# Kernel optimization log

Hardware: AMD Instinct MI355X
Metric: run time of the kernel (lower is better)

The kernel has to match this reference:

```python
import jax, jax.numpy as jnp
import numpy as np
from jax import lax

THRESHOLD = 10.0


def _conv(x, w):
    # x: [N,1,H,W], w: [O,1,kh,kw], SAME padding, stride 1 (matches nn.Conv2d with symmetric padding)
    return lax.conv_general_dilated(x, w, window_strides=(1, 1), padding='SAME',
                                    dimension_numbers=('NCHW', 'OIHW', 'NCHW'))


def _make_filters():
    # scipy.signal.gaussian(5, std=1.0): unnormalized gaussian window
    gauss = np.exp(-0.5 * ((np.arange(5) - 2.0) ** 2)).astype(np.float32)
    gauss_w = gauss.reshape(1, 1, 1, 5)  # horizontal 1x5 filter
    sobel = np.array([[1, 0, -1], [2, 0, -2], [1, 0, -1]], np.float32)
    sobel_x = sobel[None, None]  # [1,1,3,3]
    f0 = [[0, 0, 0], [0, 1, -1], [0, 0, 0]]
    f45 = [[0, 0, 0], [0, 1, 0], [0, 0, -1]]
    f90 = [[0, 0, 0], [0, 1, 0], [0, -1, 0]]
    f135 = [[0, 0, 0], [0, 1, 0], [-1, 0, 0]]
    f180 = [[0, 0, 0], [-1, 1, 0], [0, 0, 0]]
    f225 = [[-1, 0, 0], [0, 1, 0], [0, 0, 0]]
    f270 = [[0, -1, 0], [0, 1, 0], [0, 0, 0]]
    f315 = [[0, 0, -1], [0, 1, 0], [0, 0, 0]]
    dir_w = np.stack([f0, f45, f90, f135, f180, f225, f270, f315]).astype(np.float32)[:, None]  # [8,1,3,3]
    return jnp.asarray(gauss_w), jnp.asarray(sobel_x), jnp.asarray(dir_w)


def setup_inputs() -> dict:
    key = jax.random.key(0)
    B, H, W = 4, 1024, 1024
    img = jax.random.uniform(key, (B, 3, H, W), dtype=jnp.float32) * 255.0  # pixel-scale values
    gauss_w, sobel_x, dir_w = _make_filters()
    return {'img': img, 'gauss_w': gauss_w, 'sobel_x': sobel_x, 'dir_w': dir_w}


def reference(img, gauss_w, sobel_x, dir_w):
    B, C, H, W = img.shape  # C == 3
    x = img.reshape(B * 3, 1, H, W)
    # Separable gaussian blur (horizontal then vertical), all 3 channels batched together
    blurred = _conv(_conv(x, gauss_w), jnp.transpose(gauss_w, (0, 1, 3, 2)))  # [B*3,1,H,W]
    # Sobel gradients per channel
    gx = _conv(blurred, sobel_x).reshape(B, 3, H, W)
    gy = _conv(blurred, jnp.transpose(sobel_x, (0, 1, 3, 2))).reshape(B, 3, H, W)
    # Magnitude: sum of per-channel L2 magnitudes
    grad_mag = jnp.sum(jnp.sqrt(gx * gx + gy * gy), axis=1, keepdims=True)  # [B,1,H,W]
    # Orientation from summed gradients, quantized to 45-degree bins (same pi constant as original)
    grad_orientation = jnp.arctan2(gy.sum(1, keepdims=True), gx.sum(1, keepdims=True)) * (180.0 / 3.14159)
    grad_orientation = jnp.round((grad_orientation + 180.0) / 45.0) * 45.0
    # Directional differences for non-max suppression
    all_filtered = _conv(grad_mag, dir_w)  # [B,8,H,W]
    idx_pos = ((grad_orientation / 45.0) % 8).astype(jnp.int32)          # [B,1,H,W]
    idx_neg = ((grad_orientation / 45.0 + 4.0) % 8).astype(jnp.int32)
    pos = jnp.take_along_axis(all_filtered, idx_pos, axis=1)  # [B,1,H,W]
    neg = jnp.take_along_axis(all_filtered, idx_neg, axis=1)
    is_max = jnp.minimum(pos, neg) > 0.0
    thin_edges = jnp.where(is_max, grad_mag, 0.0)
    thresholded = jnp.where(thin_edges < THRESHOLD, 0.0, thin_edges)
    early_threshold = jnp.where(grad_mag < THRESHOLD, 0.0, grad_mag)
    blurred_img = blurred.reshape(B, 3, H, W)[None]  # matches torch.stack([squeeze(...)]) for B>1
    return (blurred_img, grad_mag, grad_orientation, thin_edges, thresholded, early_threshold)
```

## Files before the change

### kernel.cpp

```cpp
#include <hip/hip_runtime.h>
#include <math.h>


#define OUTW 56
#define ROWS 8
#define NT   256

struct TrigC { double c0,s0,c1,s1,c2,s2,c3,s3; };

struct ChS {
    double hA,hB,hC,hD;
    double d0,d1;
    double v0,v1;
    float  rwP;
};

__global__ __launch_bounds__(NT, 2) void canny_wave_kernel(
    const float* __restrict__ img,
    const float* __restrict__ gauss,
    float* __restrict__ out_blur,
    float* __restrict__ out_mag,
    float* __restrict__ out_ori,
    float* __restrict__ out_thin,
    float* __restrict__ out_thr,
    float* __restrict__ out_early,
    TrigC tc, int H, int W)
{
    const int lane  = threadIdx.x & 63;
    const int wid   = threadIdx.x >> 6;
    const int strip = blockIdx.x;
    const int seg   = blockIdx.y * 4 + wid;
    const int b     = blockIdx.z;

    const int  x   = strip * OUTW + lane - 4;
    const bool xin = (unsigned)x < (unsigned)W;
    const int  r0  = seg * ROWS;

    const double g0 = (double)gauss[0], g1 = (double)gauss[1], g2 = (double)gauss[2];
    const size_t cs = (size_t)H * W;
    const float* ip0 = img + (size_t)(b * 3 + 0) * cs;
    const float* ip1 = ip0 + cs;
    const float* ip2 = ip1 + cs;
    float* bp0 = out_blur + (size_t)(b * 3 + 0) * cs;
    float* bp1 = bp0 + cs;
    float* bp2 = bp1 + cs;

    const bool outok = xin && lane >= 4 && lane <= 59;

    auto rawload = [&](const float* ip, int y) -> float {
        return (xin && (unsigned)y < (unsigned)H) ? ip[(size_t)y * W + x] : 0.f;
    };
    auto hconv = [&](float rw) -> double {
        float m2 = __shfl(rw, lane - 2);
        float m1 = __shfl(rw, lane - 1);
        float p1 = __shfl(rw, lane + 1);
        float p2 = __shfl(rw, lane + 2);
        return g0 * ((double)m2 + (double)p2) + g1 * ((double)m1 + (double)p1)
             + g2 * (double)rw;
    };
    auto hinit = [&](const float* ip, ChS& s) {
        s.hA = hconv(rawload(ip, r0 - 4));
        s.hB = hconv(rawload(ip, r0 - 3));
        s.hC = hconv(rawload(ip, r0 - 2));
        s.hD = hconv(rawload(ip, r0 - 1));
        s.d0 = 0.0; s.d1 = 0.0; s.v0 = 0.0; s.v1 = 0.0;
        s.rwP = rawload(ip, r0);
    };
    auto chstep = [&](const float* ip, float* bp, ChS& s, int v,
                      double& msum, double& gxs, double& gys) {
        float  rw = s.rwP;
        s.rwP = rawload(ip, v + 3);
        double hE = hconv(rw);
        double vbn = g0 * (s.hA + hE) + g1 * (s.hB + s.hD) + g2 * s.hC;
        if (!xin || (unsigned)v >= (unsigned)H) vbn = 0.0;
        if (v >= r0 && v < r0 + ROWS && outok)
            bp[(size_t)v * W + x] = (float)vbn;
        double vbL = __shfl(vbn, lane - 1), vbR = __shfl(vbn, lane + 1);
        double dn = vbL - vbR;
        double cc = s.v0 - vbn;
        double cL = __shfl(cc, lane - 1), cR = __shfl(cc, lane + 1);
        double gx = s.d0 + 2.0 * s.d1 + dn;
        double gy = cL + 2.0 * cc + cR;
        msum += sqrt(gx * gx + gy * gy);
        gxs += gx; gys += gy;
        s.hA = s.hB; s.hB = s.hC; s.hC = s.hD; s.hD = hE;
        s.d0 = s.d1; s.d1 = dn;
        s.v0 = s.v1; s.v1 = vbn;
    };

    ChS c0s, c1s, c2s;
    hinit(ip0, c0s); hinit(ip1, c1s); hinit(ip2, c2s);

    double mg0 = 0.0, mg1 = 0.0, mgL0 = 0.0, mgL1 = 0.0, mgR0 = 0.0, mgR1 = 0.0;
    double gxp = 0.0, gyp = 0.0;
    const size_t ob = (size_t)b * cs;

    for (int v = r0 - 2; v <= r0 + ROWS + 1; ++v) {
        double msum = 0.0, gxn = 0.0, gyn = 0.0;
        chstep(ip0, bp0, c0s, v, msum, gxn, gyn);
        chstep(ip1, bp1, c1s, v, msum, gxn, gyn);
        chstep(ip2, bp2, c2s, v, msum, gxn, gyn);
        const int m = v - 1;
        const bool mv = ((unsigned)m < (unsigned)H) && xin && lane >= 3 && lane <= 60;
        double magn = mv ? msum : 0.0;
        double mgLn = __shfl(magn, lane - 1);
        double mgRn = __shfl(magn, lane + 1);

        if (v >= r0 + 2 && outok) {
            const int r = v - 2;
            double m_c = mg1;
            double gxv = gxp, gyv = gyp;

            double a = fabs(gyv);
            int n = (int)(a * tc.c0 - gxv * tc.s0 >= 0.0)
                  + (int)(a * tc.c1 - gxv * tc.s1 >= 0.0)
                  + (int)(a * tc.c2 - gxv * tc.s2 >= 0.0)
                  + (int)(a * tc.c3 - gxv * tc.s3 >= 0.0);
            int k;
            if (gyv == 0.0) {
                bool gxneg = signbit(gxv);
                k = signbit(gyv) ? (gxneg ? 0 : 4) : (gxneg ? 8 : 4);
            } else {
                k = signbit(gyv) ? 4 - n : 4 + n;
            }
            float q = 45.f * (float)k;
            if (gxv < 0.0 && fabs(gyv) < 1e-2) q = 180.f;

            int kp = k & 7;
            int dy = (int)((0x00012221u >> (kp * 4)) & 7u) - 1;
            int dx = (int)((0x21000122u >> (kp * 4)) & 7u) - 1;

            double rL = (dy < 0) ? mgL0 : (dy > 0 ? mgLn : mgL1);
            double rC = (dy < 0) ? mg0  : (dy > 0 ? magn : mg1);
            double rR = (dy < 0) ? mgR0 : (dy > 0 ? mgRn : mgR1);
            double posn = (dx < 0) ? rL : (dx > 0 ? rR : rC);
            double sL = (dy > 0) ? mgL0 : (dy < 0 ? mgLn : mgL1);
            double sC = (dy > 0) ? mg0  : (dy < 0 ? magn : mg1);
            double sR = (dy > 0) ? mgR0 : (dy < 0 ? mgRn : mgR1);
            double negn = (dx > 0) ? sL : (dx < 0 ? sR : sC);

            double pos = m_c - posn;
            double neg = m_c - negn;
            float mf = (float)m_c;
            float thin = (fmin(pos, neg) > 0.0) ? mf : 0.f;
            size_t idx = ob + (size_t)r * W + x;
            out_mag[idx]   = mf;
            out_ori[idx]   = q;
            out_thin[idx]  = thin;
            out_thr[idx]   = (thin < 10.f) ? 0.f : thin;
            out_early[idx] = (mf < 10.f) ? 0.f : mf;
        }

        mg0 = mg1; mg1 = magn;
        mgL0 = mgL1; mgL1 = mgLn;
        mgR0 = mgR1; mgR1 = mgRn;
        gxp = gxn; gyp = gyn;
    }
}

extern "C" void kernel_launch(void* const* d_in, const int* in_sizes, int n_in,
                              void* d_out, int out_size, void* d_ws, size_t ws_size,
                              hipStream_t stream) {
    const float* img   = (const float*)d_in[0];
    const float* gauss = (const float*)d_in[1];
    const int H = 1024, W = 1024;
    const int B = in_sizes[0] / (3 * H * W);

    float* out = (float*)d_out;
    const size_t cs = (size_t)H * W;
    float* out_blur  = out;
    float* out_mag   = out_blur + (size_t)B * 3 * cs;
    float* out_ori   = out_mag  + (size_t)B * cs;
    float* out_thin  = out_ori  + (size_t)B * cs;
    float* out_thr   = out_thin + (size_t)B * cs;
    float* out_early = out_thr  + (size_t)B * cs;

    const double C = 180.0 / 3.14159;
    TrigC tc;
    { double bta = 22.5 / C;  tc.c0 = cos(bta); tc.s0 = sin(bta); }
    { double bta = 67.5 / C;  tc.c1 = cos(bta); tc.s1 = sin(bta); }
    { double bta = 112.5 / C; tc.c2 = cos(bta); tc.s2 = sin(bta); }
    { double bta = 157.5 / C; tc.c3 = cos(bta); tc.s3 = sin(bta); }

    dim3 grid((W + OUTW - 1) / OUTW, H / (ROWS * 4), B);
    canny_wave_kernel<<<grid, NT, 0, stream>>>(
        img, gauss, out_blur, out_mag, out_ori, out_thin, out_thr, out_early, tc, H, W);
}
```

Baseline: 89.71 us.

## Process two adjacent pixels per lane with float2 loads and stores

Each lane now handles a horizontal pair of pixels, so a wave covers 120 output columns instead of 56. The overlapping halo work and shuffles per output pixel both shrink, and all global loads and stores become float2 vector accesses. The cost is roughly double the per-lane register state (double-precision histories for both pixels), which may hurt occupancy or cause spills. There is also a leftover redundant dn0 assignment.

```diff
diff --git a/kernel.cpp b/kernel.cpp
--- a/kernel.cpp
+++ b/kernel.cpp
@@ -2,17 +2,17 @@
 #include <math.h>
 
 
-#define OUTW 56
+#define PW   120
 #define ROWS 8
 #define NT   256
 
 struct TrigC { double c0,s0,c1,s1,c2,s2,c3,s3; };
 
 struct ChS {
-    double hA,hB,hC,hD;
-    double d0,d1;
-    double v0,v1;
-    float  rwP;
+    double hAa,hBa,hCa,hDa, hAb,hBb,hCb,hDb;
+    double d0a,d1a, d0b,d1b;
+    double v0a,v1a, v0b,v1b;
+    float  rw0,rw1;
 };
 
 __global__ __launch_bounds__(NT, 2) void canny_wave_kernel(
@@ -32,9 +32,10 @@
     const int seg   = blockIdx.y * 4 + wid;
     const int b     = blockIdx.z;
 
-    const int  x   = strip * OUTW + lane - 4;
-    const bool xin = (unsigned)x < (unsigned)W;
-    const int  r0  = seg * ROWS;
+    const int x0 = strip * PW - 4 + 2 * lane;
+    const int x1 = x0 + 1;
+    const bool pairok = (x0 >= 0) && (x1 < W);
+    const int  r0 = seg * ROWS;
 
     const double g0 = (double)gauss[0], g1 = (double)gauss[1], g2 = (double)gauss[2];
     const size_t cs = (size_t)H * W;
@@ -45,116 +46,149 @@
     float* bp1 = bp0 + cs;
     float* bp2 = bp1 + cs;
 
-    const bool outok = xin && lane >= 4 && lane <= 59;
-
-    auto rawload = [&](const float* ip, int y) -> float {
-        return (xin && (unsigned)y < (unsigned)H) ? ip[(size_t)y * W + x] : 0.f;
-    };
-    auto hconv = [&](float rw) -> double {
-        float m2 = __shfl(rw, lane - 2);
-        float m1 = __shfl(rw, lane - 1);
-        float p1 = __shfl(rw, lane + 1);
-        float p2 = __shfl(rw, lane + 2);
-        return g0 * ((double)m2 + (double)p2) + g1 * ((double)m1 + (double)p1)
-             + g2 * (double)rw;
+    const bool outok = (lane >= 2) && (lane <= 61) && ((unsigned)x0 < (unsigned)W);
+
+    auto rawload2 = [&](const float* ip, int y, float& o0, float& o1) {
+        if ((unsigned)y < (unsigned)H) {
+            if (pairok) {
+                float2 t = *reinterpret_cast<const float2*>(ip + (size_t)y * W + x0);
+                o0 = t.x; o1 = t.y;
+            } else {
+                o0 = ((unsigned)x0 < (unsigned)W) ? ip[(size_t)y * W + x0] : 0.f;
+                o1 = ((unsigned)x1 < (unsigned)W) ? ip[(size_t)y * W + x1] : 0.f;
+            }
+        } else { o0 = 0.f; o1 = 0.f; }
+    };
+    auto hpair = [&](float w0, float w1, double& hh0, double& hh1) {
+        float am0 = __shfl(w0, lane - 1), am1 = __shfl(w1, lane - 1);
+        float ap0 = __shfl(w0, lane + 1), ap1 = __shfl(w1, lane + 1);
+        hh0 = g0 * ((double)am0 + (double)ap0) + g1 * ((double)am1 + (double)w1) + g2 * (double)w0;
+        hh1 = g0 * ((double)am1 + (double)ap1) + g1 * ((double)w0 + (double)ap0) + g2 * (double)w1;
     };
     auto hinit = [&](const float* ip, ChS& s) {
-        s.hA = hconv(rawload(ip, r0 - 4));
-        s.hB = hconv(rawload(ip, r0 - 3));
-        s.hC = hconv(rawload(ip, r0 - 2));
-        s.hD = hconv(rawload(ip, r0 - 1));
-        s.d0 = 0.0; s.d1 = 0.0; s.v0 = 0.0; s.v1 = 0.0;
-        s.rwP = rawload(ip, r0);
+        float w0, w1;
+        rawload2(ip, r0 - 4, w0, w1); hpair(w0, w1, s.hAa, s.hAb);
+        rawload2(ip, r0 - 3, w0, w1); hpair(w0, w1, s.hBa, s.hBb);
+        rawload2(ip, r0 - 2, w0, w1); hpair(w0, w1, s.hCa, s.hCb);
+        rawload2(ip, r0 - 1, w0, w1); hpair(w0, w1, s.hDa, s.hDb);
+        s.d0a = s.d1a = s.d0b = s.d1b = 0.0;
+        s.v0a = s.v1a = s.v0b = s.v1b = 0.0;
+        rawload2(ip, r0, s.rw0, s.rw1);
     };
     auto chstep = [&](const float* ip, float* bp, ChS& s, int v,
-                      double& msum, double& gxs, double& gys) {
-        float  rw = s.rwP;
-        s.rwP = rawload(ip, v + 3);
-        double hE = hconv(rw);
-        double vbn = g0 * (s.hA + hE) + g1 * (s.hB + s.hD) + g2 * s.hC;
-        if (!xin || (unsigned)v >= (unsigned)H) vbn = 0.0;
-        if (v >= r0 && v < r0 + ROWS && outok)
-            bp[(size_t)v * W + x] = (float)vbn;
-        double vbL = __shfl(vbn, lane - 1), vbR = __shfl(vbn, lane + 1);
-        double dn = vbL - vbR;
-        double cc = s.v0 - vbn;
-        double cL = __shfl(cc, lane - 1), cR = __shfl(cc, lane + 1);
-        double gx = s.d0 + 2.0 * s.d1 + dn;
-        double gy = cL + 2.0 * cc + cR;
-        msum += sqrt(gx * gx + gy * gy);
-        gxs += gx; gys += gy;
-        s.hA = s.hB; s.hB = s.hC; s.hC = s.hD; s.hD = hE;
-        s.d0 = s.d1; s.d1 = dn;
-        s.v0 = s.v1; s.v1 = vbn;
+                      double& ms0, double& ms1, double& gxs0, double& gxs1,
+                      double& gys0, double& gys1) {
+        float w0 = s.rw0, w1 = s.rw1;
+        rawload2(ip, v + 3, s.rw0, s.rw1);
+        double hE0, hE1;
+        hpair(w0, w1, hE0, hE1);
+        double vb0 = g0 * (s.hAa + hE0) + g1 * (s.hBa + s.hDa) + g2 * s.hCa;
+        double vb1 = g0 * (s.hAb + hE1) + g1 * (s.hBb + s.hDb) + g2 * s.hCb;
+        if ((unsigned)v >= (unsigned)H) { vb0 = 0.0; vb1 = 0.0; }
+        if ((unsigned)x0 >= (unsigned)W) vb0 = 0.0;
+        if ((unsigned)x1 >= (unsigned)W) vb1 = 0.0;
+        if (v >= r0 && v < r0 + ROWS && outok) {
+            float2 t; t.x = (float)vb0; t.y = (float)vb1;
+            *reinterpret_cast<float2*>(bp + (size_t)v * W + x0) = t;
+        }
+        double svb1m = __shfl(vb1, lane - 1), svb0p = __shfl(vb0, lane + 1);
+        double dn0 = svb1m - vb0 * 0.0 - vb1;
+        dn0 = svb1m - vb1;
+        double dn1 = vb0 - svb0p;
+        double cc0 = s.v0a - vb0, cc1 = s.v0b - vb1;
+        double scc1m = __shfl(cc1, lane - 1), scc0p = __shfl(cc0, lane + 1);
+        double gx0 = s.d0a + 2.0 * s.d1a + dn0;
+        double gx1 = s.d0b + 2.0 * s.d1b + dn1;
+        double gy0 = scc1m + 2.0 * cc0 + cc1;
+        double gy1 = cc0 + 2.0 * cc1 + scc0p;
+        ms0 += sqrt(gx0 * gx0 + gy0 * gy0);
+        ms1 += sqrt(gx1 * gx1 + gy1 * gy1);
+        gxs0 += gx0; gys0 += gy0; gxs1 += gx1; gys1 += gy1;
+        s.hAa = s.hBa; s.hBa = s.hCa; s.hCa = s.hDa; s.hDa = hE0;
+        s.hAb = s.hBb; s.hBb = s.hCb; s.hCb = s.hDb; s.hDb = hE1;
+        s.d0a = s.d1a; s.d1a = dn0;  s.d0b = s.d1b; s.d1b = dn1;
+        s.v0a = s.v1a; s.v1a = vb0;  s.v0b = s.v1b; s.v1b = vb1;
     };
 
     ChS c0s, c1s, c2s;
     hinit(ip0, c0s); hinit(ip1, c1s); hinit(ip2, c2s);
 
-    double mg0 = 0.0, mg1 = 0.0, mgL0 = 0.0, mgL1 = 0.0, mgR0 = 0.0, mgR1 = 0.0;
-    double gxp = 0.0, gyp = 0.0;
+    double R0a = 0.0, R0b = 0.0, R0L = 0.0, R0R = 0.0;
+    double R1a = 0.0, R1b = 0.0, R1L = 0.0, R1R = 0.0;
+    double gxp0 = 0.0, gyp0 = 0.0, gxp1 = 0.0, gyp1 = 0.0;
     const size_t ob = (size_t)b * cs;
 
     for (int v = r0 - 2; v <= r0 + ROWS + 1; ++v) {
-        double msum = 0.0, gxn = 0.0, gyn = 0.0;
-        chstep(ip0, bp0, c0s, v, msum, gxn, gyn);
-        chstep(ip1, bp1, c1s, v, msum, gxn, gyn);
-        chstep(ip2, bp2, c2s, v, msum, gxn, gyn);
-        const int m = v - 1;
-        const bool mv = ((unsigned)m < (unsigned)H) && xin && lane >= 3 && lane <= 60;
-        double magn = mv ? msum : 0.0;
-        double mgLn = __shfl(magn, lane - 1);
-        double mgRn = __shfl(magn, lane + 1);
+        double ms0 = 0.0, ms1 = 0.0, gxn0 = 0.0, gxn1 = 0.0, gyn0 = 0.0, gyn1 = 0.0;
+        chstep(ip0, bp0, c0s, v, ms0, ms1, gxn0, gxn1, gyn0, gyn1);
+        chstep(ip1, bp1, c1s, v, ms0, ms1, gxn0, gxn1, gyn0, gyn1);
+        chstep(ip2, bp2, c2s, v, ms0, ms1, gxn0, gxn1, gyn0, gyn1);
+        const bool okrow = ((unsigned)(v - 1) < (unsigned)H);
+        double m0n = (okrow && (unsigned)x0 < (unsigned)W && lane >= 2 && lane <= 62) ? ms0 : 0.0;
+        double m1n = (okrow && (unsigned)x1 < (unsigned)W && lane >= 1 && lane <= 61) ? ms1 : 0.0;
+        double mLn = __shfl(m1n, lane - 1);
+        double mRn = __shfl(m0n, lane + 1);
 
         if (v >= r0 + 2 && outok) {
             const int r = v - 2;
-            double m_c = mg1;
-            double gxv = gxp, gyv = gyp;
-
-            double a = fabs(gyv);
-            int n = (int)(a * tc.c0 - gxv * tc.s0 >= 0.0)
-                  + (int)(a * tc.c1 - gxv * tc.s1 >= 0.0)
-                  + (int)(a * tc.c2 - gxv * tc.s2 >= 0.0)
-                  + (int)(a * tc.c3 - gxv * tc.s3 >= 0.0);
-            int k;
-            if (gyv == 0.0) {
-                bool gxneg = signbit(gxv);
-                k = signbit(gyv) ? (gxneg ? 0 : 4) : (gxneg ? 8 : 4);
-            } else {
-                k = signbit(gyv) ? 4 - n : 4 + n;
+            float2 w_mag, w_ori, w_thin, w_thr, w_early;
+#pragma unroll 2
+            for (int px = 0; px < 2; ++px) {
+                double gxv = px ? gxp1 : gxp0;
+                double gyv = px ? gyp1 : gyp0;
+                double m_c = px ? R1b : R1a;
+                double u0L = px ? R0a : R0L, u0C = px ? R0b : R0a, u0R = px ? R0R : R0b;
+                double u1L = px ? R1a : R1L, u1C = px ? R1b : R1a, u1R = px ? R1R : R1b;
+                double unL = px ? m0n : mLn, unC = px ? m1n : m0n, unR = px ? mRn : m1n;
+
+                double a = fabs(gyv);
+                int n = (int)(a * tc.c0 - gxv * tc.s0 >= 0.0)
+                      + (int)(a * tc.c1 - gxv * tc.s1 >= 0.0)
+                      + (int)(a * tc.c2 - gxv * tc.s2 >= 0.0)
+                      + (int)(a * tc.c3 - gxv * tc.s3 >= 0.0);
+                int k;
+                if (gyv == 0.0) {
+                    bool gxneg = signbit(gxv);
+                    k = signbit(gyv) ? (gxneg ? 0 : 4) : (gxneg ? 8 : 4);
+                } else {
+                    k = signbit(gyv) ? 4 - n : 4 + n;
+                }
+                float q = 45.f * (float)k;
+                if (gxv < 0.0 && fabs(gyv) < 1e-2) q = 180.f;
+
+                int kp = k & 7;
+                int dy = (int)((0x00012221u >> (kp * 4)) & 7u) - 1;
+                int dx = (int)((0x21000122u >> (kp * 4)) & 7u) - 1;
+
+                double rL = (dy < 0) ? u0L : (dy > 0 ? unL : u1L);
+                double rC = (dy < 0) ? u0C : (dy > 0 ? unC : u1C);
+                double rR = (dy < 0) ? u0R : (dy > 0 ? unR : u1R);
+                double posn = (dx < 0) ? rL : (dx > 0 ? rR : rC);
+                double sL = (dy > 0) ? u0L : (dy < 0 ? unL : u1L);
+                double sC = (dy > 0) ? u0C : (dy < 0 ? unC : u1C);
+                double sR = (dy > 0) ? u0R : (dy < 0 ? unR : u1R);
+                double negn = (dx > 0) ? sL : (dx < 0 ? sR : sC);
+
+                double pos = m_c - posn;
+                double neg = m_c - negn;
+                float mf = (float)m_c;
+                float thin = (fmin(pos, neg) > 0.0) ? mf : 0.f;
+                float thrv = (thin < 10.f) ? 0.f : thin;
+                float earl = (mf < 10.f) ? 0.f : mf;
+                if (px == 0) { w_mag.x = mf; w_ori.x = q; w_thin.x = thin; w_thr.x = thrv; w_early.x = earl; }
+                else         { w_mag.y = mf; w_ori.y = q; w_thin.y = thin; w_thr.y = thrv; w_early.y = earl; }
             }
-            float q = 45.f * (float)k;
-            if (gxv < 0.0 && fabs(gyv) < 1e-2) q = 180.f;
-
-            int kp = k & 7;
-            int dy = (int)((0x00012221u >> (kp * 4)) & 7u) - 1;
-            int dx = (int)((0x21000122u >> (kp * 4)) & 7u) - 1;
-
-            double rL = (dy < 0) ? mgL0 : (dy > 0 ? mgLn : mgL1);
-            double rC = (dy < 0) ? mg0  : (dy > 0 ? magn : mg1);
-            double rR = (dy < 0) ? mgR0 : (dy > 0 ? mgRn : mgR1);
-            double posn = (dx < 0) ? rL : (dx > 0 ? rR : rC);
-            double sL = (dy > 0) ? mgL0 : (dy < 0 ? mgLn : mgL1);
-            double sC = (dy > 0) ? mg0  : (dy < 0 ? magn : mg1);
-            double sR = (dy > 0) ? mgR0 : (dy < 0 ? mgRn : mgR1);
-            double negn = (dx > 0) ? sL : (dx < 0 ? sR : sC);
-
-            double pos = m_c - posn;
-            double neg = m_c - negn;
-            float mf = (float)m_c;
-            float thin = (fmin(pos, neg) > 0.0) ? mf : 0.f;
-            size_t idx = ob + (size_t)r * W + x;
-            out_mag[idx]   = mf;
-            out_ori[idx]   = q;
-            out_thin[idx]  = thin;
-            out_thr[idx]   = (thin < 10.f) ? 0.f : thin;
-            out_early[idx] = (mf < 10.f) ? 0.f : mf;
+            size_t idx = ob + (size_t)r * W + x0;
+            *reinterpret_cast<float2*>(out_mag   + idx) = w_mag;
+            *reinterpret_cast<float2*>(out_ori   + idx) = w_ori;
+            *reinterpret_cast<float2*>(out_thin  + idx) = w_thin;
+            *reinterpret_cast<float2*>(out_thr   + idx) = w_thr;
+            *reinterpret_cast<float2*>(out_early + idx) = w_early;
         }
 
-        mg0 = mg1; mg1 = magn;
-        mgL0 = mgL1; mgL1 = mgLn;
-        mgR0 = mgR1; mgR1 = mgRn;
-        gxp = gxn; gyp = gyn;
+        R0a = R1a; R0b = R1b; R0L = R1L; R0R = R1R;
+        R1a = m0n; R1b = m1n; R1L = mLn; R1R = mRn;
+        gxp0 = gxn0; gyp0 = gyn0; gxp1 = gxn1; gyp1 = gyn1;
     }
 }
 
@@ -182,7 +216,7 @@
     { double bta = 112.5 / C; tc.c2 = cos(bta); tc.s2 = sin(bta); }
     { double bta = 157.5 / C; tc.c3 = cos(bta); tc.s3 = sin(bta); }
 
-    dim3 grid((W + OUTW - 1) / OUTW, H / (ROWS * 4), B);
+    dim3 grid((W + PW - 1) / PW, H / (ROWS * 4), B);
     canny_wave_kernel<<<grid, NT, 0, stream>>>(
         img, gauss, out_blur, out_mag, out_ori, out_thin, out_thr, out_early, tc, H, W);
 }
```

New measurement: 96.24 us. 7.3% more time.
